# Kernel tuning notes

Measured on AMD Instinct MI355X. Metric: run time of the kernel, lower is better.

The kernel has to match this reference:

```python
import jax, jax.numpy as jnp
import numpy as np

DIM = 512
HEADS = 8
B, H, W = 8, 32, 32
SMOOTH = 1e-4
BN_EPS = 1e-5


def _conv(x, w, pad):
    return jax.lax.conv_general_dilated(
        x, w, window_strides=(1, 1), padding=[(pad, pad), (pad, pad)],
        dimension_numbers=('NCHW', 'OIHW', 'NCHW'))


def setup_inputs() -> dict:
    key = jax.random.key(0)
    k1, k2, k3 = jax.random.split(key, 3)
    x = jax.random.normal(k1, (B, DIM, H, W), dtype=jnp.float32)
    # conv weights with fan-in style scaling for stable magnitudes
    W_qkv = jax.random.normal(k2, (3 * DIM, DIM, 3, 3), dtype=jnp.float32) * (1.0 / np.sqrt(DIM * 9))
    W_out = jax.random.normal(k3, (DIM, DIM, 1, 1), dtype=jnp.float32) * (1.0 / np.sqrt(DIM))
    gamma = jnp.ones((DIM,), dtype=jnp.float32)
    beta = jnp.zeros((DIM,), dtype=jnp.float32)
    return {"x": x, "W_qkv": W_qkv, "W_out": W_out, "gamma": gamma, "beta": beta}


def reference(x, W_qkv, W_out, gamma, beta):
    b, c, h, w = x.shape
    g = HEADS
    d = c // g
    n = h * w
    qkv = _conv(x, W_qkv, pad=1)                      # [b, 3c, h, w]
    q, k, v = jnp.split(qkv, 3, axis=1)
    # 'b (g d) h w -> b g (h w) d'
    to_seq = lambda t: t.reshape(b, g, d, n).transpose(0, 1, 3, 2)
    q, k, v = to_seq(q), to_seq(k), to_seq(v)         # [b, g, n, d]
    attn = jnp.einsum('bgid,bgjd->bgij', q, k)        # [b, g, n, n]
    qn = jnp.sqrt(jnp.sum(q * q, axis=-1) + SMOOTH)   # [b, g, n]
    kn = jnp.sqrt(jnp.sum(k * k, axis=-1) + SMOOTH)   # [b, g, n]
    attn = attn / (qn[:, :, :, None] * kn[:, :, None, :] + SMOOTH)
    out = jnp.einsum('bgij,bgjd->bgid', attn, v)      # [b, g, n, d]
    # 'b g (h w) d -> b (g d) h w'
    out = out.transpose(0, 1, 3, 2).reshape(b, c, h, w)
    out = _conv(out, W_out, pad=0)
    # BatchNorm2d (training mode: batch statistics, biased variance)
    mean = jnp.mean(out, axis=(0, 2, 3))
    var = jnp.var(out, axis=(0, 2, 3))
    out = (out - mean[None, :, None, None]) * jax.lax.rsqrt(var + BN_EPS)[None, :, None, None]
    out = out * gamma[None, :, None, None] + beta[None, :, None, None]
    return jax.nn.relu(out)
```

## Files before the change

kernel.cpp:

```cpp
#include <hip/hip_runtime.h>
#include <math.h>


#define SMOOTH 1e-4f
#define BN_EPS 1e-5f

typedef __attribute__((ext_vector_type(8))) short bf16x8;
typedef __attribute__((ext_vector_type(8))) unsigned short u16x8;
typedef __attribute__((ext_vector_type(4))) float f32x4;
typedef __attribute__((ext_vector_type(4))) unsigned int u32x4;
typedef __attribute__((ext_vector_type(4))) unsigned short u16x4;

__device__ inline unsigned short bf16rne(float f) {
  unsigned int u = __float_as_uint(f);
  u += 0x7fff + ((u >> 16) & 1);
  return (unsigned short)(u >> 16);
}
__device__ inline float b2f(unsigned short u) {
  return __uint_as_float((unsigned int)u << 16);
}

typedef __attribute__((address_space(1))) void gvoid;
typedef __attribute__((address_space(3))) void lvoid;
__device__ __forceinline__ void async16(const void* g, void* l) {
  __builtin_amdgcn_global_load_lds((gvoid*)g, (lvoid*)l, 16, 0, 0);
}

__global__ void repack_w(const float* __restrict__ wq,
                         unsigned short* __restrict__ wqr2) {
  __shared__ float Ws[2304];
  const int tid = threadIdx.x;
  const size_t pair0 = (size_t)blockIdx.x * 256;
  for (int off = tid; off < 576; off += 256)
    *(float4*)(Ws + off * 4) = *(const float4*)(wq + pair0 * 9 + off * 4);
  __syncthreads();
  const int co = (int)(pair0 >> 9);
  const int ciBase = (int)(pair0 & 511);
  const int cotile = co >> 6, co_l = co & 63;
  for (int idx = tid; idx < 288; idx += 256) {
    int t = idx >> 5;
    int oct = idx & 31;
    int ci = ciBase + oct * 8;
    int ci0c = ci >> 5, c4 = oct & 3;
    u16x8 pk;
#pragma unroll
    for (int e = 0; e < 8; ++e) pk[e] = bf16rne(Ws[(oct * 8 + e) * 9 + t]);
    size_t o = (size_t)(ci0c * 24 + cotile) * 18432 +
               (size_t)((c4 * 9 + t) * 64 + co_l) * 8;
    *(u16x8*)(wqr2 + o) = pk;
  }
}

__global__ void repack_x(const float* __restrict__ x,
                         unsigned short* __restrict__ xrp2) {
  __shared__ float Xs[64 * 132];
  const int tid = threadIdx.x;
  const int p0 = (blockIdx.x & 7) * 128;
  const int ci0 = ((blockIdx.x >> 3) & 7) * 64;
  const int b = blockIdx.x >> 6;
  for (int k = 0; k < 8; ++k) {
    int idx = tid + k * 256;
    int c4 = idx & 31, row = idx >> 5;
    *(float4*)(Xs + row * 132 + c4 * 4) =
        *(const float4*)(x + ((size_t)(b * 512 + ci0 + row)) * 1024 + p0 + c4 * 4);
  }
  __syncthreads();
  const int pl = tid >> 1, half = tid & 1;
  const int p = p0 + pl;
  const int h = p >> 5, w = p & 31;
#pragma unroll
  for (int v = 0; v < 8; ++v) {
    u16x4 pk;
#pragma unroll
    for (int e = 0; e < 4; ++e)
      pk[e] = bf16rne(Xs[(half * 32 + v * 4 + e) * 132 + pl]);
    int cc = ci0 + half * 32 + v * 4;
    int ci0c = cc >> 5, c4 = (cc >> 3) & 3, e0 = cc & 7;
    size_t gran = (size_t)((ci0c * 4 + c4) * 8 + b) * 1156 + (h + 1) * 34 + (w + 1);
    *(u16x4*)(xrp2 + gran * 8 + e0) = pk;
  }
}

__global__ void repack_wo(const float* __restrict__ wo,
                          unsigned short* __restrict__ wor,
                          float* __restrict__ sums, float* __restrict__ sumsq) {
  int idx = blockIdx.x * 256 + threadIdx.x;
  wor[idx] = bf16rne(wo[idx]);
  if (blockIdx.x < 2) {
    sums[idx] = 0.f;
    sumsq[idx] = 0.f;
  }
}

__global__ __launch_bounds__(256) void conv3x3_mfma(
    const unsigned short* __restrict__ wqr2,
    const unsigned short* __restrict__ xrp2,
    unsigned short* __restrict__ qt, unsigned short* __restrict__ kt,
    unsigned short* __restrict__ vt, float* __restrict__ rqn,
    float* __restrict__ rkn) {
  __shared__ __align__(16) unsigned short Wl[2304 * 8];
  __shared__ __align__(16) unsigned short Xl[4 * 256 * 8];
  __shared__ float Snl[128];

  const int tid = threadIdx.x;
  const int lane = tid & 63;
  const int wave = tid >> 6;
  const int wco = (wave & 1) * 32;
  const int wn = (wave >> 1) * 64;
  const int l15 = lane & 15;
  const int quad = lane >> 4;
  const int h0 = blockIdx.x * 4;
  const int co0 = blockIdx.y * 64;
  const int b = blockIdx.z;

  f32x4 acc[2][4];
  for (int ma = 0; ma < 2; ++ma)
    for (int nb = 0; nb < 4; ++nb) acc[ma][nb] = (f32x4){0.f, 0.f, 0.f, 0.f};

  for (int ci0 = 0; ci0 < 512; ci0 += 32) {
    const int ci0c = ci0 >> 5;
    __syncthreads();
    const unsigned short* wsrc =
        wqr2 + (size_t)(ci0c * 24 + (co0 >> 6)) * 18432;
    {
      int cbase = wave * 9;
#pragma unroll
      for (int j = 0; j < 9; ++j) {
        int c = cbase + j;
        async16(wsrc + (size_t)c * 512 + lane * 8, Wl + (size_t)c * 512);
      }
    }
    const unsigned short* xsrc =
        xrp2 + ((size_t)((ci0c * 4 + wave) * 8 + b) * 1156 + h0 * 34) * 8;
#pragma unroll
    for (int j = 0; j < 4; ++j)
      async16(xsrc + (size_t)j * 512 + lane * 8,
              Xl + (size_t)(wave * 256 + j * 64) * 8);
    __syncthreads();

#pragma unroll
    for (int t = 0; t < 9; ++t) {
      const int ky = t / 3, kx = t - ky * 3;
      bf16x8 af[2], bfr[4];
#pragma unroll
      for (int ma = 0; ma < 2; ++ma)
        af[ma] = *(const bf16x8*)(
            Wl + (size_t)((quad * 9 + t) * 64 + wco + ma * 16 + l15) * 8);
#pragma unroll
      for (int nb = 0; nb < 4; ++nb) {
        int n = wn + nb * 16 + l15;
        int hh = (n >> 5) + ky;
        int wi = (n & 31) + kx;
        bfr[nb] = *(const bf16x8*)(Xl + (size_t)(quad * 256 + hh * 34 + wi) * 8);
      }
#pragma unroll
      for (int ma = 0; ma < 2; ++ma)
#pragma unroll
        for (int nb = 0; nb < 4; ++nb)
          acc[ma][nb] = __builtin_amdgcn_mfma_f32_16x16x32_bf16(
              af[ma], bfr[nb], acc[ma][nb], 0, 0, 0);
    }
  }

  const int sec = co0 >> 9;
  const int g = (co0 & 511) >> 6;
  const int bg = b * 8 + g;
  if (sec < 2) {
    unsigned short* dst = (sec == 0) ? qt : kt;
#pragma unroll
    for (int ma = 0; ma < 2; ++ma)
#pragma unroll
      for (int nb = 0; nb < 4; ++nb) {
        int n = wn + nb * 16 + l15;
        int p = (h0 + (n >> 5)) * 32 + (n & 31);
        int db = wco + ma * 16 + quad * 4;
        u16x4 pk;
#pragma unroll
        for (int r = 0; r < 4; ++r) pk[r] = bf16rne(acc[ma][nb][r]);
        *(u16x4*)(dst + ((size_t)bg * 1024 + p) * 64 + db) = pk;
      }
    float ps[4];
#pragma unroll
    for (int nb = 0; nb < 4; ++nb) {
      float s = 0.f;
#pragma unroll
      for (int ma = 0; ma < 2; ++ma)
#pragma unroll
        for (int r = 0; r < 4; ++r) s = fmaf(acc[ma][nb][r], acc[ma][nb][r], s);
      s += __shfl_down(s, 32);
      s += __shfl_down(s, 16);
      ps[nb] = s;
    }
    if (wco == 0 && quad == 0)
#pragma unroll
      for (int nb = 0; nb < 4; ++nb) Snl[wn + nb * 16 + l15] = ps[nb];
    __syncthreads();
    if (wco == 32 && quad == 0) {
      float* ndst = (sec == 0) ? rqn : rkn;
#pragma unroll
      for (int nb = 0; nb < 4; ++nb) {
        int n = wn + nb * 16 + l15;
        int p = (h0 + (n >> 5)) * 32 + (n & 31);
        ndst[bg * 1024 + p] = rsqrtf(Snl[n] + ps[nb] + SMOOTH);
      }
    }
  } else {
#pragma unroll
    for (int ma = 0; ma < 2; ++ma)
#pragma unroll
      for (int nb = 0; nb < 4; ++nb) {
        int n = wn + nb * 16 + l15;
        int p = (h0 + (n >> 5)) * 32 + (n & 31);
#pragma unroll
        for (int r = 0; r < 4; ++r) {
          int d = wco + ma * 16 + quad * 4 + r;
          vt[((size_t)bg * 64 + d) * 1024 + p] = bf16rne(acc[ma][nb][r]);
        }
      }
  }
}

__global__ __launch_bounds__(256) void attn_mfma(
    const unsigned short* __restrict__ qt, const unsigned short* __restrict__ kt,
    const unsigned short* __restrict__ vt, const float* __restrict__ rqn,
    const float* __restrict__ rkn, unsigned short* __restrict__ aob) {
  __shared__ __align__(16) unsigned short Kl[64 * 72];
  __shared__ __align__(16) unsigned short Vl[64 * 72];
  __shared__ __align__(16) unsigned short Sl[64 * 72];

  const int tid = threadIdx.x;
  const int lane = tid & 63, wave = tid >> 6;
  const int l15 = lane & 15, quad = lane >> 4;
  const int bg = blockIdx.x;
  const int i0 = blockIdx.y * 64;
  const int iw = i0 + wave * 16;
  const int b = bg >> 3, g = bg & 7;

  bf16x8 qf[2];
#pragma unroll
  for (int ks = 0; ks < 2; ++ks)
    qf[ks] = *(const bf16x8*)(
        qt + ((size_t)bg * 1024 + iw + l15) * 64 + ks * 32 + quad * 8);

  float rq[4];
#pragma unroll
  for (int r = 0; r < 4; ++r) rq[r] = rqn[bg * 1024 + iw + quad * 4 + r];

  f32x4 oacc[4];
  for (int nf = 0; nf < 4; ++nf) oacc[nf] = (f32x4){0.f, 0.f, 0.f, 0.f};

  unsigned short* Sw = Sl + wave * 16 * 72;

  for (int jt = 0; jt < 16; ++jt) {
    const int j0 = jt * 64;
    __syncthreads();
    for (int idx = tid; idx < 512; idx += 256) {
      int c8 = idx & 7, row = idx >> 3;
      *(u32x4*)(Kl + row * 72 + c8 * 8) =
          *(const u32x4*)(kt + ((size_t)bg * 1024 + j0 + row) * 64 + c8 * 8);
      *(u32x4*)(Vl + row * 72 + c8 * 8) =
          *(const u32x4*)(vt + ((size_t)bg * 64 + row) * 1024 + j0 + c8 * 8);
    }
    __syncthreads();

    f32x4 sacc[4];
    for (int nb = 0; nb < 4; ++nb) sacc[nb] = (f32x4){0.f, 0.f, 0.f, 0.f};
#pragma unroll
    for (int ks = 0; ks < 2; ++ks) {
#pragma unroll
      for (int nb = 0; nb < 4; ++nb) {
        bf16x8 kf = *(const bf16x8*)(Kl + (l15 + 16 * nb) * 72 + ks * 32 + quad * 8);
        sacc[nb] = __builtin_amdgcn_mfma_f32_16x16x32_bf16(
            qf[ks], kf, sacc[nb], 0, 0, 0);
      }
    }

#pragma unroll
    for (int nb = 0; nb < 4; ++nb) {
      float rk = rkn[bg * 1024 + j0 + l15 + 16 * nb];
#pragma unroll
      for (int r = 0; r < 4; ++r) {
        float s = sacc[nb][r] * (rq[r] * rk);
        Sw[(quad * 4 + r) * 72 + l15 + 16 * nb] = bf16rne(s);
      }
    }
#pragma unroll
    for (int ks2 = 0; ks2 < 2; ++ks2) {
      bf16x8 sa = *(const bf16x8*)(Sw + l15 * 72 + ks2 * 32 + quad * 8);
#pragma unroll
      for (int nf = 0; nf < 4; ++nf) {
        bf16x8 vb = *(const bf16x8*)(Vl + (l15 + 16 * nf) * 72 + ks2 * 32 + quad * 8);
        oacc[nf] = __builtin_amdgcn_mfma_f32_16x16x32_bf16(sa, vb, oacc[nf], 0, 0, 0);
      }
    }
  }

#pragma unroll
  for (int nf = 0; nf < 4; ++nf)
#pragma unroll
    for (int r = 0; r < 4; ++r) {
      int i = iw + quad * 4 + r;
      int d = l15 + 16 * nf;
      aob[((size_t)(b * 1024) + i) * 512 + g * 64 + d] = bf16rne(oacc[nf][r]);
    }
}

__global__ __launch_bounds__(256) void conv1x1_mfma(
    const unsigned short* __restrict__ wor, const unsigned short* __restrict__ aob,
    unsigned short* __restrict__ yb, float* __restrict__ sums,
    float* __restrict__ sumsq) {
  __shared__ __align__(16) unsigned short Wl[64 * 40];
  __shared__ __align__(16) unsigned short Bl[64 * 40];

  const int tid = threadIdx.x;
  const int lane = tid & 63, wave = tid >> 6;
  const int l15 = lane & 15, quad = lane >> 4;
  const int wco = (wave & 1) * 32;
  const int wp = (wave >> 1) * 32;
  const int p0 = blockIdx.x * 64;
  const int co0 = blockIdx.y * 64;
  const int b = blockIdx.z;

  f32x4 acc[2][2];
  for (int ma = 0; ma < 2; ++ma)
    for (int nb = 0; nb < 2; ++nb) acc[ma][nb] = (f32x4){0.f, 0.f, 0.f, 0.f};

  for (int ci0 = 0; ci0 < 512; ci0 += 32) {
    __syncthreads();
    {
      int c4 = tid & 3, co = tid >> 2;
      *(u32x4*)(Wl + co * 40 + c4 * 8) =
          *(const u32x4*)(wor + (size_t)(co0 + co) * 512 + ci0 + c4 * 8);
      *(u32x4*)(Bl + co * 40 + c4 * 8) =
          *(const u32x4*)(aob + ((size_t)(b * 1024) + p0 + co) * 512 + ci0 + c4 * 8);
    }
    __syncthreads();

    bf16x8 af[2], bf[2];
#pragma unroll
    for (int ma = 0; ma < 2; ++ma)
      af[ma] = *(const bf16x8*)(Wl + (wco + ma * 16 + l15) * 40 + quad * 8);
#pragma unroll
    for (int nb = 0; nb < 2; ++nb)
      bf[nb] = *(const bf16x8*)(Bl + (wp + nb * 16 + l15) * 40 + quad * 8);
#pragma unroll
    for (int ma = 0; ma < 2; ++ma)
#pragma unroll
      for (int nb = 0; nb < 2; ++nb)
        acc[ma][nb] = __builtin_amdgcn_mfma_f32_16x16x32_bf16(
            af[ma], bf[nb], acc[ma][nb], 0, 0, 0);
  }

#pragma unroll
  for (int ma = 0; ma < 2; ++ma)
#pragma unroll
    for (int r = 0; r < 4; ++r) {
      int co = co0 + wco + ma * 16 + quad * 4 + r;
      float s1 = 0.f, s2 = 0.f;
#pragma unroll
      for (int nb = 0; nb < 2; ++nb) {
        float v = acc[ma][nb][r];
        yb[((size_t)(b * 512) + co) * 1024 + p0 + wp + nb * 16 + l15] = bf16rne(v);
        s1 += v;
        s2 = fmaf(v, v, s2);
      }
      for (int off = 8; off >= 1; off >>= 1) {
        s1 += __shfl_down(s1, off, 16);
        s2 += __shfl_down(s2, off, 16);
      }
      if (l15 == 0) {
        atomicAdd(&sums[co], s1);
        atomicAdd(&sumsq[co], s2);
      }
    }
}

__global__ void bn_kernel(const unsigned short* __restrict__ yb,
                          const float* __restrict__ sums,
                          const float* __restrict__ sumsq,
                          const float* __restrict__ gamma,
                          const float* __restrict__ beta,
                          float* __restrict__ out) {
  int idx = blockIdx.x * 256 + threadIdx.x;
  int c = (idx >> 8) & 511;
  u16x4 vb = *(const u16x4*)(yb + (size_t)idx * 4);
  float mean = sums[c] * (1.f / 8192.f);
  float var = sumsq[c] * (1.f / 8192.f) - mean * mean;
  float sc = gamma[c] * rsqrtf(var + BN_EPS);
  float sh = beta[c] - mean * sc;
  float4 r;
  r.x = fmaxf(0.f, fmaf(b2f(vb[0]), sc, sh));
  r.y = fmaxf(0.f, fmaf(b2f(vb[1]), sc, sh));
  r.z = fmaxf(0.f, fmaf(b2f(vb[2]), sc, sh));
  r.w = fmaxf(0.f, fmaf(b2f(vb[3]), sc, sh));
  ((float4*)out)[idx] = r;
}

extern "C" void kernel_launch(void* const* d_in, const int* in_sizes, int n_in,
                              void* d_out, int out_size, void* d_ws,
                              size_t ws_size, hipStream_t stream) {
  const float* x = (const float*)d_in[0];
  const float* wq = (const float*)d_in[1];
  const float* wo = (const float*)d_in[2];
  const float* gamma = (const float*)d_in[3];
  const float* beta = (const float*)d_in[4];
  float* out = (float*)d_out;

  unsigned short* qt = (unsigned short*)d_ws;
  unsigned short* kt = qt + (size_t)4194304;
  unsigned short* vt = kt + (size_t)4194304;
  unsigned short* aob = vt + (size_t)4194304;
  unsigned short* wqr2 = aob + (size_t)4194304;
  unsigned short* wor = wqr2 + (size_t)7077888;
  unsigned short* xrp2 = wor + (size_t)262144;
  float* rqn = (float*)(xrp2 + (size_t)4736000);
  float* rkn = rqn + 65536;
  unsigned short* yb = (unsigned short*)(rkn + 65536);
  float* sums = (float*)(yb + (size_t)4194304);
  float* sumsq = sums + 512;

  hipMemsetAsync(xrp2, 0, (size_t)4736000 * 2, stream);
  repack_w<<<dim3(3072), 256, 0, stream>>>(wq, wqr2);
  repack_x<<<dim3(512), 256, 0, stream>>>(x, xrp2);
  repack_wo<<<dim3(1024), 256, 0, stream>>>(wo, wor, sums, sumsq);
  conv3x3_mfma<<<dim3(8, 24, 8), 256, 0, stream>>>(wqr2, xrp2, qt, kt, vt, rqn, rkn);
  attn_mfma<<<dim3(64, 16), 256, 0, stream>>>(qt, kt, vt, rqn, rkn, aob);
  conv1x1_mfma<<<dim3(16, 8, 8), 256, 0, stream>>>(wor, aob, yb, sums, sumsq);
  bn_kernel<<<dim3(4096), 256, 0, stream>>>(yb, sums, sumsq, gamma, beta, out);
}
```

Before: 293.4 us.

## Retile 3x3 conv to 32x32x16 MFMA with 8-row tiles and fuse prep kernels

The three repack kernels are merged into one launch that dispatches on block index, which removes two kernel launches. The 3x3 conv now covers 8 output rows per block instead of 4, so each weight tile loaded to LDS is reused across twice as many pixels. Each wave owns all 64 output channels for 64 pixels and uses 32x32x16 bf16 MFMA instead of 16x16x32. Because a wave now holds every channel, the per-pixel norm reduction needs only a shuffle, so the LDS exchange and its extra barrier are gone. The cost is half as many blocks (768), which lowers parallelism, and larger accumulator tiles that raise register pressure.

```diff
diff --git a/kernel.cpp b/kernel.cpp
--- a/kernel.cpp
+++ b/kernel.cpp
@@ -8,6 +8,7 @@
 typedef __attribute__((ext_vector_type(8))) short bf16x8;
 typedef __attribute__((ext_vector_type(8))) unsigned short u16x8;
 typedef __attribute__((ext_vector_type(4))) float f32x4;
+typedef __attribute__((ext_vector_type(16))) float f32x16;
 typedef __attribute__((ext_vector_type(4))) unsigned int u32x4;
 typedef __attribute__((ext_vector_type(4))) unsigned short u16x4;
 
@@ -26,69 +27,72 @@
   __builtin_amdgcn_global_load_lds((gvoid*)g, (lvoid*)l, 16, 0, 0);
 }
 
-__global__ void repack_w(const float* __restrict__ wq,
-                         unsigned short* __restrict__ wqr2) {
-  __shared__ float Ws[2304];
+__global__ void prep_kernel(const float* __restrict__ wq,
+                            unsigned short* __restrict__ wqr2,
+                            const float* __restrict__ x,
+                            unsigned short* __restrict__ xrp2,
+                            const float* __restrict__ wo,
+                            unsigned short* __restrict__ wor,
+                            float* __restrict__ sums,
+                            float* __restrict__ sumsq) {
+  __shared__ float Sh[64 * 132];
   const int tid = threadIdx.x;
-  const size_t pair0 = (size_t)blockIdx.x * 256;
-  for (int off = tid; off < 576; off += 256)
-    *(float4*)(Ws + off * 4) = *(const float4*)(wq + pair0 * 9 + off * 4);
-  __syncthreads();
-  const int co = (int)(pair0 >> 9);
-  const int ciBase = (int)(pair0 & 511);
-  const int cotile = co >> 6, co_l = co & 63;
-  for (int idx = tid; idx < 288; idx += 256) {
-    int t = idx >> 5;
-    int oct = idx & 31;
-    int ci = ciBase + oct * 8;
-    int ci0c = ci >> 5, c4 = oct & 3;
-    u16x8 pk;
-#pragma unroll
-    for (int e = 0; e < 8; ++e) pk[e] = bf16rne(Ws[(oct * 8 + e) * 9 + t]);
-    size_t o = (size_t)(ci0c * 24 + cotile) * 18432 +
-               (size_t)((c4 * 9 + t) * 64 + co_l) * 8;
-    *(u16x8*)(wqr2 + o) = pk;
-  }
-}
-
-__global__ void repack_x(const float* __restrict__ x,
-                         unsigned short* __restrict__ xrp2) {
-  __shared__ float Xs[64 * 132];
-  const int tid = threadIdx.x;
-  const int p0 = (blockIdx.x & 7) * 128;
-  const int ci0 = ((blockIdx.x >> 3) & 7) * 64;
-  const int b = blockIdx.x >> 6;
-  for (int k = 0; k < 8; ++k) {
-    int idx = tid + k * 256;
-    int c4 = idx & 31, row = idx >> 5;
-    *(float4*)(Xs + row * 132 + c4 * 4) =
-        *(const float4*)(x + ((size_t)(b * 512 + ci0 + row)) * 1024 + p0 + c4 * 4);
-  }
-  __syncthreads();
-  const int pl = tid >> 1, half = tid & 1;
-  const int p = p0 + pl;
-  const int h = p >> 5, w = p & 31;
-#pragma unroll
-  for (int v = 0; v < 8; ++v) {
-    u16x4 pk;
-#pragma unroll
-    for (int e = 0; e < 4; ++e)
-      pk[e] = bf16rne(Xs[(half * 32 + v * 4 + e) * 132 + pl]);
-    int cc = ci0 + half * 32 + v * 4;
-    int ci0c = cc >> 5, c4 = (cc >> 3) & 3, e0 = cc & 7;
-    size_t gran = (size_t)((ci0c * 4 + c4) * 8 + b) * 1156 + (h + 1) * 34 + (w + 1);
-    *(u16x4*)(xrp2 + gran * 8 + e0) = pk;
-  }
-}
-
-__global__ void repack_wo(const float* __restrict__ wo,
-                          unsigned short* __restrict__ wor,
-                          float* __restrict__ sums, float* __restrict__ sumsq) {
-  int idx = blockIdx.x * 256 + threadIdx.x;
-  wor[idx] = bf16rne(wo[idx]);
-  if (blockIdx.x < 2) {
-    sums[idx] = 0.f;
-    sumsq[idx] = 0.f;
+  const int bid = blockIdx.x;
+  if (bid < 3072) {
+    const size_t pair0 = (size_t)bid * 256;
+    for (int off = tid; off < 576; off += 256)
+      *(float4*)(Sh + off * 4) = *(const float4*)(wq + pair0 * 9 + off * 4);
+    __syncthreads();
+    const int co = (int)(pair0 >> 9);
+    const int ciBase = (int)(pair0 & 511);
+    const int cotile = co >> 6, co_l = co & 63;
+    for (int idx = tid; idx < 288; idx += 256) {
+      int t = idx >> 5;
+      int oct = idx & 31;
+      int ci = ciBase + oct * 8;
+      int ci0c = ci >> 5, c4 = oct & 3;
+      u16x8 pk;
+#pragma unroll
+      for (int e = 0; e < 8; ++e) pk[e] = bf16rne(Sh[(oct * 8 + e) * 9 + t]);
+      size_t o = (size_t)(ci0c * 24 + cotile) * 18432 +
+                 (size_t)((c4 * 9 + t) * 64 + co_l) * 8;
+      *(u16x8*)(wqr2 + o) = pk;
+    }
+  } else if (bid < 3584) {
+    const int bx = bid - 3072;
+    const int p0 = (bx & 7) * 128;
+    const int ci0 = ((bx >> 3) & 7) * 64;
+    const int b = bx >> 6;
+    for (int k = 0; k < 8; ++k) {
+      int idx = tid + k * 256;
+      int c4 = idx & 31, row = idx >> 5;
+      *(float4*)(Sh + row * 132 + c4 * 4) =
+          *(const float4*)(x + ((size_t)(b * 512 + ci0 + row)) * 1024 + p0 + c4 * 4);
+    }
+    __syncthreads();
+    const int pl = tid >> 1, half = tid & 1;
+    const int p = p0 + pl;
+    const int h = p >> 5, w = p & 31;
+#pragma unroll
+    for (int v = 0; v < 8; ++v) {
+      u16x4 pk;
+#pragma unroll
+      for (int e = 0; e < 4; ++e)
+        pk[e] = bf16rne(Sh[(half * 32 + v * 4 + e) * 132 + pl]);
+      int cc = ci0 + half * 32 + v * 4;
+      int ci0c = cc >> 5, c4 = (cc >> 3) & 3, e0 = cc & 7;
+      size_t gran =
+          (size_t)((ci0c * 4 + c4) * 8 + b) * 1156 + (h + 1) * 34 + (w + 1);
+      *(u16x4*)(xrp2 + gran * 8 + e0) = pk;
+    }
+  } else {
+    const int rb = bid - 3584;
+    int idx = rb * 256 + tid;
+    wor[idx] = bf16rne(wo[idx]);
+    if (rb < 2) {
+      sums[idx] = 0.f;
+      sumsq[idx] = 0.f;
+    }
   }
 }
 
@@ -99,66 +103,69 @@
     unsigned short* __restrict__ vt, float* __restrict__ rqn,
     float* __restrict__ rkn) {
   __shared__ __align__(16) unsigned short Wl[2304 * 8];
-  __shared__ __align__(16) unsigned short Xl[4 * 256 * 8];
-  __shared__ float Snl[128];
+  __shared__ __align__(16) unsigned short Xl[1360 * 8];
 
   const int tid = threadIdx.x;
   const int lane = tid & 63;
   const int wave = tid >> 6;
-  const int wco = (wave & 1) * 32;
-  const int wn = (wave >> 1) * 64;
-  const int l15 = lane & 15;
-  const int quad = lane >> 4;
-  const int h0 = blockIdx.x * 4;
+  const int l31 = lane & 31;
+  const int hi = lane >> 5;
+  const int wn = wave * 64;
+  const int h0 = blockIdx.x * 8;
   const int co0 = blockIdx.y * 64;
   const int b = blockIdx.z;
 
-  f32x4 acc[2][4];
+  f32x16 acc[2][2];
   for (int ma = 0; ma < 2; ++ma)
-    for (int nb = 0; nb < 4; ++nb) acc[ma][nb] = (f32x4){0.f, 0.f, 0.f, 0.f};
+    for (int nbt = 0; nbt < 2; ++nbt)
+#pragma unroll
+      for (int e = 0; e < 16; ++e) acc[ma][nbt][e] = 0.f;
 
   for (int ci0 = 0; ci0 < 512; ci0 += 32) {
     const int ci0c = ci0 >> 5;
     __syncthreads();
-    const unsigned short* wsrc =
-        wqr2 + (size_t)(ci0c * 24 + (co0 >> 6)) * 18432;
-    {
-      int cbase = wave * 9;
-#pragma unroll
-      for (int j = 0; j < 9; ++j) {
-        int c = cbase + j;
-        async16(wsrc + (size_t)c * 512 + lane * 8, Wl + (size_t)c * 512);
-      }
+    const unsigned short* wsrc = wqr2 + (size_t)(ci0c * 24 + (co0 >> 6)) * 18432;
+#pragma unroll
+    for (int j = 0; j < 9; ++j) {
+      int c = wave * 9 + j;
+      async16(wsrc + (size_t)c * 512 + lane * 8, Wl + (size_t)c * 512);
     }
     const unsigned short* xsrc =
         xrp2 + ((size_t)((ci0c * 4 + wave) * 8 + b) * 1156 + h0 * 34) * 8;
 #pragma unroll
-    for (int j = 0; j < 4; ++j)
+    for (int j = 0; j < 5; ++j)
       async16(xsrc + (size_t)j * 512 + lane * 8,
-              Xl + (size_t)(wave * 256 + j * 64) * 8);
+              Xl + (size_t)(wave * 340 + j * 64) * 8);
+    async16(xsrc + (size_t)276 * 8 + lane * 8, Xl + (size_t)(wave * 340 + 276) * 8);
     __syncthreads();
 
 #pragma unroll
     for (int t = 0; t < 9; ++t) {
       const int ky = t / 3, kx = t - ky * 3;
-      bf16x8 af[2], bfr[4];
-#pragma unroll
-      for (int ma = 0; ma < 2; ++ma)
-        af[ma] = *(const bf16x8*)(
-            Wl + (size_t)((quad * 9 + t) * 64 + wco + ma * 16 + l15) * 8);
-#pragma unroll
-      for (int nb = 0; nb < 4; ++nb) {
-        int n = wn + nb * 16 + l15;
-        int hh = (n >> 5) + ky;
-        int wi = (n & 31) + kx;
-        bfr[nb] = *(const bf16x8*)(Xl + (size_t)(quad * 256 + hh * 34 + wi) * 8);
-      }
-#pragma unroll
-      for (int ma = 0; ma < 2; ++ma)
-#pragma unroll
-        for (int nb = 0; nb < 4; ++nb)
-          acc[ma][nb] = __builtin_amdgcn_mfma_f32_16x16x32_bf16(
-              af[ma], bfr[nb], acc[ma][nb], 0, 0, 0);
+      bf16x8 af[2][2], bfr[2][2];
+#pragma unroll
+      for (int s = 0; s < 2; ++s) {
+        const int pl = (s * 2 + hi);
+#pragma unroll
+        for (int ma = 0; ma < 2; ++ma)
+          af[ma][s] = *(const bf16x8*)(
+              Wl + (size_t)(pl * 576 + t * 64 + ma * 32 + l31) * 8);
+#pragma unroll
+        for (int nbt = 0; nbt < 2; ++nbt) {
+          int n = wn + nbt * 32 + l31;
+          int hh = (n >> 5) + ky;
+          int wi = (n & 31) + kx;
+          bfr[nbt][s] = *(const bf16x8*)(Xl + (size_t)(pl * 340 + hh * 34 + wi) * 8);
+        }
+      }
+#pragma unroll
+      for (int s = 0; s < 2; ++s)
+#pragma unroll
+        for (int ma = 0; ma < 2; ++ma)
+#pragma unroll
+          for (int nbt = 0; nbt < 2; ++nbt)
+            acc[ma][nbt] = __builtin_amdgcn_mfma_f32_32x32x16_bf16(
+                af[ma][s], bfr[nbt][s], acc[ma][nbt], 0, 0, 0);
     }
   }
 
@@ -170,51 +177,50 @@
 #pragma unroll
     for (int ma = 0; ma < 2; ++ma)
 #pragma unroll
-      for (int nb = 0; nb < 4; ++nb) {
-        int n = wn + nb * 16 + l15;
+      for (int nbt = 0; nbt < 2; ++nbt) {
+        int n = wn + nbt * 32 + l31;
         int p = (h0 + (n >> 5)) * 32 + (n & 31);
-        int db = wco + ma * 16 + quad * 4;
-        u16x4 pk;
-#pragma unroll
-        for (int r = 0; r < 4; ++r) pk[r] = bf16rne(acc[ma][nb][r]);
-        *(u16x4*)(dst + ((size_t)bg * 1024 + p) * 64 + db) = pk;
-      }
-    float ps[4];
-#pragma unroll
-    for (int nb = 0; nb < 4; ++nb) {
+#pragma unroll
+        for (int g4 = 0; g4 < 4; ++g4) {
+          u16x4 pk;
+#pragma unroll
+          for (int r2 = 0; r2 < 4; ++r2) pk[r2] = bf16rne(acc[ma][nbt][g4 * 4 + r2]);
+          int d = ma * 32 + g4 * 8 + hi * 4;
+          *(u16x4*)(dst + ((size_t)bg * 1024 + p) * 64 + d) = pk;
+        }
+      }
+    float sn[2];
+#pragma unroll
+    for (int nbt = 0; nbt < 2; ++nbt) {
       float s = 0.f;
 #pragma unroll
       for (int ma = 0; ma < 2; ++ma)
 #pragma unroll
-        for (int r = 0; r < 4; ++r) s = fmaf(acc[ma][nb][r], acc[ma][nb][r], s);
+        for (int e = 0; e < 16; ++e)
+          s = fmaf(acc[ma][nbt][e], acc[ma][nbt][e], s);
       s += __shfl_down(s, 32);
-      s += __shfl_down(s, 16);
-      ps[nb] = s;
-    }
-    if (wco == 0 && quad == 0)
-#pragma unroll
-      for (int nb = 0; nb < 4; ++nb) Snl[wn + nb * 16 + l15] = ps[nb];
-    __syncthreads();
-    if (wco == 32 && quad == 0) {
+      sn[nbt] = s;
+    }
+    if (lane < 32) {
       float* ndst = (sec == 0) ? rqn : rkn;
 #pragma unroll
-      for (int nb = 0; nb < 4; ++nb) {
-        int n = wn + nb * 16 + l15;
+      for (int nbt = 0; nbt < 2; ++nbt) {
+        int n = wn + nbt * 32 + lane;
         int p = (h0 + (n >> 5)) * 32 + (n & 31);
-        ndst[bg * 1024 + p] = rsqrtf(Snl[n] + ps[nb] + SMOOTH);
+        ndst[bg * 1024 + p] = rsqrtf(sn[nbt] + SMOOTH);
       }
     }
   } else {
 #pragma unroll
     for (int ma = 0; ma < 2; ++ma)
 #pragma unroll
-      for (int nb = 0; nb < 4; ++nb) {
-        int n = wn + nb * 16 + l15;
+      for (int nbt = 0; nbt < 2; ++nbt) {
+        int n = wn + nbt * 32 + l31;
         int p = (h0 + (n >> 5)) * 32 + (n & 31);
 #pragma unroll
-        for (int r = 0; r < 4; ++r) {
-          int d = wco + ma * 16 + quad * 4 + r;
-          vt[((size_t)bg * 64 + d) * 1024 + p] = bf16rne(acc[ma][nb][r]);
+        for (int reg = 0; reg < 16; ++reg) {
+          int d = ma * 32 + (reg & 3) + 8 * (reg >> 2) + 4 * hi;
+          vt[((size_t)bg * 64 + d) * 1024 + p] = bf16rne(acc[ma][nbt][reg]);
         }
       }
   }
@@ -420,10 +426,10 @@
   float* sumsq = sums + 512;
 
   hipMemsetAsync(xrp2, 0, (size_t)4736000 * 2, stream);
-  repack_w<<<dim3(3072), 256, 0, stream>>>(wq, wqr2);
-  repack_x<<<dim3(512), 256, 0, stream>>>(x, xrp2);
-  repack_wo<<<dim3(1024), 256, 0, stream>>>(wo, wor, sums, sumsq);
-  conv3x3_mfma<<<dim3(8, 24, 8), 256, 0, stream>>>(wqr2, xrp2, qt, kt, vt, rqn, rkn);
+  prep_kernel<<<dim3(4608), 256, 0, stream>>>(wq, wqr2, x, xrp2, wo, wor, sums,
+                                              sumsq);
+  conv3x3_mfma<<<dim3(4, 24, 8), 256, 0, stream>>>(wqr2, xrp2, qt, kt, vt, rqn,
+                                                   rkn);
   attn_mfma<<<dim3(64, 16), 256, 0, stream>>>(qt, kt, vt, rqn, rkn, aob);
   conv1x1_mfma<<<dim3(16, 8, 8), 256, 0, stream>>>(wor, aob, yb, sums, sumsq);
   bn_kernel<<<dim3(4096), 256, 0, stream>>>(yb, sums, sumsq, gamma, beta, out);
```

After: 294.2 us. No clear change (+0.3%).
